# Optimization experiments

Hardware: AMD Instinct MI355X
Metric: run time of the kernel (lower is better)

Reference implementation:

```python
import jax, jax.numpy as jnp
import numpy as np

B, S, D, H, E = 2, 2048, 1024, 2048, 8
TOP_K = 2
AUX_COEF = 0.01


def setup_inputs() -> dict:
    key = jax.random.key(0)
    ks = jax.random.split(key, 5)
    x = jax.random.normal(ks[0], (B, S, D), jnp.float32)
    Wr = jax.random.normal(ks[1], (E, D), jnp.float32) * 0.02   # router: Linear(D, E) weight [E, D]
    W1 = jax.random.normal(ks[2], (E, H, D), jnp.float32) * 0.02  # per-expert Linear(D, H)
    W2 = jax.random.normal(ks[3], (E, D, H), jnp.float32) * 0.02  # per-expert Linear(H, D)
    W3 = jax.random.normal(ks[4], (E, H, D), jnp.float32) * 0.02  # per-expert Linear(D, H)
    return {"x": x, "Wr": Wr, "W1": W1, "W2": W2, "W3": W3}


def reference(x, Wr, W1, W2, W3):
    b, s, d = x.shape
    e = Wr.shape[0]
    xf = x.reshape(-1, d)                               # [N, D]
    logits = xf @ Wr.T                                  # [N, E]
    probs = jax.nn.softmax(logits, axis=-1)
    _, topk_idx = jax.lax.top_k(logits, TOP_K)          # indices from logits (as in torch code)
    topk_probs, _ = jax.lax.top_k(probs, TOP_K)         # values from probs (same order; softmax monotone)
    # aux loss: density of top-1 expert * mean router prob
    density = jnp.mean(jax.nn.one_hot(topk_idx[:, 0], e, dtype=xf.dtype), axis=0)
    aux_loss = AUX_COEF * jnp.sum(density * probs.mean(axis=0)) * e
    # combine gates: gate[n, j] = sum_i topk_probs[n,i] * 1[topk_idx[n,i]==j]
    gates = jnp.sum(jax.nn.one_hot(topk_idx, e, dtype=xf.dtype) * topk_probs[..., None], axis=1)  # [N, E]
    # dense per-expert SwiGLU; masked combine gives identical math to gather/scatter loop
    h = jax.nn.silu(jnp.einsum('nd,ehd->enh', xf, W1)) * jnp.einsum('nd,ehd->enh', xf, W3)  # [E, N, H]
    y = jnp.einsum('enh,edh->end', h, W2)               # [E, N, D]
    out = jnp.einsum('ne,end->nd', gates, y)            # [N, D]
    return out.reshape(b, s, d), aux_loss
```

## Files before the change

kernel.cpp:

```cpp
#include <hip/hip_runtime.h>
#include <stdint.h>

#define NTOK 4096
#define DD 1024
#define HH 2048
#define NE 8
#define CAP 4096

typedef short bf16x8 __attribute__((ext_vector_type(8)));
typedef float f32x4 __attribute__((ext_vector_type(4)));
typedef unsigned short u16;
typedef unsigned int u32;

__device__ __forceinline__ u16 f2b(float f){
    union { float f; u32 u; } v; v.f = f;
    return (u16)((v.u + 0x7fffu + ((v.u >> 16) & 1u)) >> 16);
}
__device__ __forceinline__ u32 pk2(float a, float b){
    return (u32)f2b(a) | ((u32)f2b(b) << 16);
}
__device__ __forceinline__ void gload16(const u16* g, u16* l){
    __builtin_amdgcn_global_load_lds((const __attribute__((address_space(1))) u32*)g,
                                     (__attribute__((address_space(3))) u32*)l, 16, 0, 0);
}

__global__ __launch_bounds__(256) void cvt_w_kernel(const float* __restrict__ W1,
        const float* __restrict__ W2, const float* __restrict__ W3,
        u16* __restrict__ w1b, u16* __restrict__ w2b, u16* __restrict__ w3b){
    int y = blockIdx.y;
    const float* s; u16* d;
    if (y == 0){ s = W1; d = w1b; }
    else if (y == 1){ s = W2; d = w2b; }
    else { s = W3; d = w3b; }
    int i = blockIdx.x * 256 + threadIdx.x;
    float4 v = reinterpret_cast<const float4*>(s)[i];
    ushort4 o; o.x = f2b(v.x); o.y = f2b(v.y); o.z = f2b(v.z); o.w = f2b(v.w);
    reinterpret_cast<ushort4*>(d)[i] = o;
}

__global__ __launch_bounds__(256) void router_kernel(const float* __restrict__ x,
                              const float* __restrict__ Wr,
                              int* __restrict__ cnt, int* __restrict__ list,
                              float* __restrict__ glist, float* __restrict__ psum,
                              int* __restrict__ cnt1, int* __restrict__ islot,
                              u16* __restrict__ xb){
    __shared__ float wS[NE * DD];
    __shared__ float psumS[NE];
    __shared__ int cnt1S[NE], cntS[NE], baseS[NE];
    __shared__ int tE[32], tL[32];
    __shared__ float tP[32];
    int tid = threadIdx.x;
    for (int i = tid; i < NE * DD / 4; i += 256)
        reinterpret_cast<float4*>(wS)[i] = reinterpret_cast<const float4*>(Wr)[i];
    if (tid < NE){ psumS[tid] = 0.f; cnt1S[tid] = 0; cntS[tid] = 0; }
    __syncthreads();
    int lane = tid & 63, w = tid >> 6;
    for (int t = 0; t < 4; ++t){
        int li = w * 4 + t;
        int n = blockIdx.x * 16 + li;
        const float4* xr = reinterpret_cast<const float4*>(x + (size_t)n * DD);
        ushort4* xbr = reinterpret_cast<ushort4*>(xb + (size_t)n * DD);
        float acc[NE];
        #pragma unroll
        for (int e = 0; e < NE; ++e) acc[e] = 0.f;
        #pragma unroll
        for (int j = 0; j < 4; ++j){
            float4 xv = xr[lane + 64 * j];
            ushort4 xo; xo.x = f2b(xv.x); xo.y = f2b(xv.y); xo.z = f2b(xv.z); xo.w = f2b(xv.w);
            xbr[lane + 64 * j] = xo;
            #pragma unroll
            for (int e = 0; e < NE; ++e){
                float4 wv = reinterpret_cast<const float4*>(wS + e * DD)[lane + 64 * j];
                acc[e] += xv.x * wv.x + xv.y * wv.y + xv.z * wv.z + xv.w * wv.w;
            }
        }
        #pragma unroll
        for (int e = 0; e < NE; ++e){
            float v = acc[e];
            #pragma unroll
            for (int s = 32; s > 0; s >>= 1) v += __shfl_xor(v, s);
            acc[e] = v;
        }
        if (lane == 0){
            float mx = acc[0];
            #pragma unroll
            for (int e = 1; e < NE; ++e) mx = fmaxf(mx, acc[e]);
            float p[NE], sm = 0.f;
            #pragma unroll
            for (int e = 0; e < NE; ++e){ p[e] = expf(acc[e] - mx); sm += p[e]; }
            float inv = 1.f / sm;
            #pragma unroll
            for (int e = 0; e < NE; ++e){ p[e] *= inv; atomicAdd(&psumS[e], p[e]); }
            int i0 = 0;
            #pragma unroll
            for (int e = 1; e < NE; ++e) if (acc[e] > acc[i0]) i0 = e;
            int i1 = -1;
            #pragma unroll
            for (int e = 0; e < NE; ++e) if (e != i0 && (i1 < 0 || acc[e] > acc[i1])) i1 = e;
            atomicAdd(&cnt1S[i0], 1);
            int l0 = atomicAdd(&cntS[i0], 1);
            int l1 = atomicAdd(&cntS[i1], 1);
            tE[li * 2] = i0; tE[li * 2 + 1] = i1;
            tP[li * 2] = p[i0]; tP[li * 2 + 1] = p[i1];
            tL[li * 2] = l0; tL[li * 2 + 1] = l1;
        }
    }
    __syncthreads();
    if (tid < NE){
        baseS[tid] = atomicAdd(&cnt[tid], cntS[tid]);
        atomicAdd(&psum[tid], psumS[tid]);
        atomicAdd(&cnt1[tid], cnt1S[tid]);
    }
    __syncthreads();
    if (tid < 32){
        int e = tE[tid], pos = baseS[e] + tL[tid];
        int n = blockIdx.x * 16 + (tid >> 1);
        list[e * CAP + pos]  = n;
        glist[e * CAP + pos] = tP[tid];
        islot[n * 2 + (tid & 1)] = e * CAP + pos;
    }
}

__global__ void finalize_kernel(const int* __restrict__ cnt, int* __restrict__ offs,
                                const float* __restrict__ psum, const int* __restrict__ cnt1,
                                float* __restrict__ aux_out){
    if (threadIdx.x == 0 && blockIdx.x == 0){
        int o = 0; float aux = 0.f;
        for (int e = 0; e < NE; ++e){
            offs[e] = o; o += cnt[e];
            aux += ((float)cnt1[e] * (1.f / NTOK)) * (psum[e] * (1.f / NTOK));
        }
        aux_out[0] = 0.01f * aux * (float)NE;
    }
}

__global__ __launch_bounds__(256, 3) void ffn1_kernel(const u16* __restrict__ xb,
        const u16* __restrict__ w1b, const u16* __restrict__ w3b,
        const int* __restrict__ cnt, const int* __restrict__ offs,
        const int* __restrict__ list, u16* __restrict__ hbuf){
    int bid = blockIdx.x;
    int widx = (bid & 7) * 1024 + (bid >> 3);
    int e = widx >> 10, n0t = (widx >> 5) & 31, mt = widx & 31;
    int rows = cnt[e];
    int m0 = mt * 128;
    if (m0 >= rows) return;
    int n0 = n0t * 64;

    __shared__ u16 aS[128 * 64];
    __shared__ u16 bS[128 * 64];

    int tid = threadIdx.x, lane = tid & 63, w = tid >> 6;
    int wm = (w & 1) * 64, wn = (w >> 1) * 32;
    int fr = lane & 15, fg = lane >> 4, fr7 = fr & 7;
    int rc = lane >> 3, ce = ((lane & 7) ^ rc) * 8;

    const u16* aptr[4];
    const u16* bptr[4];
    #pragma unroll
    for (int q = 0; q < 4; ++q){
        int r = m0 + (w * 4 + q) * 8 + rc;
        int tok = list[e * CAP + (r < rows ? r : rows - 1)];
        aptr[q] = xb + (size_t)tok * DD + ce;
        int br = (w * 4 + q) * 8 + rc;
        const u16* wb = (br < 64) ? w1b : w3b;
        bptr[q] = wb + ((size_t)e * HH + n0 + (br & 63)) * DD + ce;
    }
    u16* aL = aS + w * 4 * 512;
    u16* bL = bS + w * 4 * 512;

    f32x4 acc1[4][2], acc3[4][2];
    #pragma unroll
    for (int mi = 0; mi < 4; ++mi)
        #pragma unroll
        for (int ni = 0; ni < 2; ++ni)
            #pragma unroll
            for (int j = 0; j < 4; ++j){ acc1[mi][ni][j] = 0.f; acc3[mi][ni][j] = 0.f; }

    for (int k0 = 0; k0 < DD; k0 += 64){
        #pragma unroll
        for (int q = 0; q < 4; ++q){
            gload16(aptr[q] + k0, aL + q * 512);
            gload16(bptr[q] + k0, bL + q * 512);
        }
        __syncthreads();
        #pragma unroll
        for (int ks = 0; ks < 2; ++ks){
            int sl = ((ks * 4 + fg) ^ fr7) * 8;
            bf16x8 a[4], b1[2], b3[2];
            #pragma unroll
            for (int mi = 0; mi < 4; ++mi)
                a[mi] = *reinterpret_cast<const bf16x8*>(&aS[(wm + mi * 16 + fr) * 64 + sl]);
            #pragma unroll
            for (int ni = 0; ni < 2; ++ni){
                b1[ni] = *reinterpret_cast<const bf16x8*>(&bS[(wn + ni * 16 + fr) * 64 + sl]);
                b3[ni] = *reinterpret_cast<const bf16x8*>(&bS[(64 + wn + ni * 16 + fr) * 64 + sl]);
            }
            #pragma unroll
            for (int mi = 0; mi < 4; ++mi)
                #pragma unroll
                for (int ni = 0; ni < 2; ++ni){
                    acc1[mi][ni] = __builtin_amdgcn_mfma_f32_16x16x32_bf16(a[mi], b1[ni], acc1[mi][ni], 0, 0, 0);
                    acc3[mi][ni] = __builtin_amdgcn_mfma_f32_16x16x32_bf16(a[mi], b3[ni], acc3[mi][ni], 0, 0, 0);
                }
        }
        __syncthreads();
    }

    int hoff = offs[e];
    #pragma unroll
    for (int mi = 0; mi < 4; ++mi)
        #pragma unroll
        for (int ni = 0; ni < 2; ++ni)
            #pragma unroll
            for (int j = 0; j < 4; ++j){
                int r = wm + mi * 16 + fg * 4 + j;
                int tr = m0 + r;
                if (tr < rows){
                    int c = n0 + wn + ni * 16 + fr;
                    float v1 = acc1[mi][ni][j], v3 = acc3[mi][ni][j];
                    float hv = (v1 / (1.f + expf(-v1))) * v3;
                    hbuf[(size_t)(hoff + tr) * HH + c] = f2b(hv);
                }
            }
}

__global__ __launch_bounds__(256, 3) void ffn2_kernel(const u16* __restrict__ hbuf,
        const u16* __restrict__ w2b, const int* __restrict__ cnt,
        const int* __restrict__ offs, float* __restrict__ ybuf){
    int bid = blockIdx.x;
    int widx = (bid & 7) * 256 + (bid >> 3);
    int e = widx >> 8, n0t = (widx >> 5) & 7, mt = widx & 31;
    int rows = cnt[e];
    int m0 = mt * 128;
    if (m0 >= rows) return;
    int n0 = n0t * 128;

    __shared__ u16 aS[128 * 64];
    __shared__ u16 bS[128 * 64];

    int tid = threadIdx.x, lane = tid & 63, w = tid >> 6;
    int wm = (w & 1) * 64, wn = (w >> 1) * 64;
    int fr = lane & 15, fg = lane >> 4, fr7 = fr & 7;
    int rc = lane >> 3, ce = ((lane & 7) ^ rc) * 8;

    int hoff = offs[e];
    const u16* aptr[4];
    #pragma unroll
    for (int q = 0; q < 4; ++q){
        int r = m0 + (w * 4 + q) * 8 + rc;
        if (r >= rows) r = rows - 1;
        aptr[q] = hbuf + (size_t)(hoff + r) * HH + ce;
    }
    const u16* bp = w2b + ((size_t)e * DD + n0 + w * 32 + rc) * HH + ce;
    u16* aL = aS + w * 4 * 512;
    u16* bL = bS + w * 4 * 512;

    f32x4 acc[4][4];
    #pragma unroll
    for (int mi = 0; mi < 4; ++mi)
        #pragma unroll
        for (int ni = 0; ni < 4; ++ni)
            #pragma unroll
            for (int j = 0; j < 4; ++j) acc[mi][ni][j] = 0.f;

    for (int k0 = 0; k0 < HH; k0 += 64){
        #pragma unroll
        for (int q = 0; q < 4; ++q){
            gload16(aptr[q] + k0, aL + q * 512);
            gload16(bp + q * 8 * HH + k0, bL + q * 512);
        }
        __syncthreads();
        #pragma unroll
        for (int ks = 0; ks < 2; ++ks){
            int sl = ((ks * 4 + fg) ^ fr7) * 8;
            bf16x8 a[4], b[4];
            #pragma unroll
            for (int mi = 0; mi < 4; ++mi)
                a[mi] = *reinterpret_cast<const bf16x8*>(&aS[(wm + mi * 16 + fr) * 64 + sl]);
            #pragma unroll
            for (int ni = 0; ni < 4; ++ni)
                b[ni] = *reinterpret_cast<const bf16x8*>(&bS[(wn + ni * 16 + fr) * 64 + sl]);
            #pragma unroll
            for (int mi = 0; mi < 4; ++mi)
                #pragma unroll
                for (int ni = 0; ni < 4; ++ni)
                    acc[mi][ni] = __builtin_amdgcn_mfma_f32_16x16x32_bf16(a[mi], b[ni], acc[mi][ni], 0, 0, 0);
        }
        __syncthreads();
    }

    #pragma unroll
    for (int mi = 0; mi < 4; ++mi)
        #pragma unroll
        for (int ni = 0; ni < 4; ++ni)
            #pragma unroll
            for (int j = 0; j < 4; ++j){
                int r = wm + mi * 16 + fg * 4 + j;
                int tr = m0 + r;
                if (tr < rows){
                    int c = wn + ni * 16 + fr;
                    ybuf[(size_t)(hoff + tr) * DD + n0 + c] = acc[mi][ni][j];
                }
            }
}

__global__ __launch_bounds__(256, 2) void ffn1_small(const u16* __restrict__ xb,
        const float* __restrict__ W1f, const float* __restrict__ W3f,
        const int* __restrict__ cnt, const int* __restrict__ offs,
        const int* __restrict__ list, u16* __restrict__ hbuf){
    int bid = blockIdx.x;
    int widx = (bid & 7) * 512 + (bid >> 3);
    int e = widx >> 9, n0t = (widx >> 5) & 15, mt = widx & 31;
    int rows = cnt[e];
    int m0 = mt * 128;
    if (m0 >= rows) return;
    int n0 = n0t * 128;
    __shared__ u16 aS[128 * 64];
    __shared__ u16 b1S[128 * 64];
    __shared__ u16 b3S[128 * 64];
    int tid = threadIdx.x, lane = tid & 63, w = tid >> 6;
    int wm = (w & 1) * 64, wn = (w >> 1) * 64;
    int fr = lane & 15, fg = lane >> 4, fr7 = fr & 7;
    int rc = lane >> 3, ce = ((lane & 7) ^ rc) * 8;
    const u16* aptr[4];
    #pragma unroll
    for (int q = 0; q < 4; ++q){
        int r = m0 + (w * 4 + q) * 8 + rc;
        int tok = list[e * CAP + (r < rows ? r : rows - 1)];
        aptr[q] = xb + (size_t)tok * DD + ce;
    }
    size_t brw = (size_t)(e * HH + n0 + w * 32 + rc) * DD + ce;
    const float* b1pf = W1f + brw;
    const float* b3pf = W3f + brw;
    u16* aL  = aS  + w * 4 * 512;
    u16* b1L = b1S + w * 4 * 512;
    u16* b3L = b3S + w * 4 * 512;
    f32x4 acc1[4][4], acc3[4][4];
    #pragma unroll
    for (int mi = 0; mi < 4; ++mi)
        #pragma unroll
        for (int ni = 0; ni < 4; ++ni)
            #pragma unroll
            for (int j = 0; j < 4; ++j){ acc1[mi][ni][j] = 0.f; acc3[mi][ni][j] = 0.f; }
    for (int k0 = 0; k0 < DD; k0 += 64){
        #pragma unroll
        for (int q = 0; q < 4; ++q){
            gload16(aptr[q] + k0, aL + q * 512);
            const float* s1 = b1pf + q * 8 * DD + k0;
            float4 f0 = reinterpret_cast<const float4*>(s1)[0];
            float4 f1 = reinterpret_cast<const float4*>(s1)[1];
            int4 v; v.x = pk2(f0.x,f0.y); v.y = pk2(f0.z,f0.w); v.z = pk2(f1.x,f1.y); v.w = pk2(f1.z,f1.w);
            *reinterpret_cast<int4*>(b1L + q * 512 + lane * 8) = v;
            const float* s3 = b3pf + q * 8 * DD + k0;
            float4 g0 = reinterpret_cast<const float4*>(s3)[0];
            float4 g1 = reinterpret_cast<const float4*>(s3)[1];
            int4 u; u.x = pk2(g0.x,g0.y); u.y = pk2(g0.z,g0.w); u.z = pk2(g1.x,g1.y); u.w = pk2(g1.z,g1.w);
            *reinterpret_cast<int4*>(b3L + q * 512 + lane * 8) = u;
        }
        __syncthreads();
        #pragma unroll
        for (int ks = 0; ks < 2; ++ks){
            int sl = ((ks * 4 + fg) ^ fr7) * 8;
            bf16x8 a[4], b1[4], b3[4];
            #pragma unroll
            for (int mi = 0; mi < 4; ++mi)
                a[mi] = *reinterpret_cast<const bf16x8*>(&aS[(wm + mi * 16 + fr) * 64 + sl]);
            #pragma unroll
            for (int ni = 0; ni < 4; ++ni){
                b1[ni] = *reinterpret_cast<const bf16x8*>(&b1S[(wn + ni * 16 + fr) * 64 + sl]);
                b3[ni] = *reinterpret_cast<const bf16x8*>(&b3S[(wn + ni * 16 + fr) * 64 + sl]);
            }
            #pragma unroll
            for (int mi = 0; mi < 4; ++mi)
                #pragma unroll
                for (int ni = 0; ni < 4; ++ni){
                    acc1[mi][ni] = __builtin_amdgcn_mfma_f32_16x16x32_bf16(a[mi], b1[ni], acc1[mi][ni], 0, 0, 0);
                    acc3[mi][ni] = __builtin_amdgcn_mfma_f32_16x16x32_bf16(a[mi], b3[ni], acc3[mi][ni], 0, 0, 0);
                }
        }
        __syncthreads();
    }
    int hoff = offs[e];
    #pragma unroll
    for (int mi = 0; mi < 4; ++mi)
        #pragma unroll
        for (int ni = 0; ni < 4; ++ni)
            #pragma unroll
            for (int j = 0; j < 4; ++j){
                int r = wm + mi * 16 + fg * 4 + j;
                int tr = m0 + r;
                if (tr < rows){
                    int c = wn + ni * 16 + fr;
                    float v1 = acc1[mi][ni][j], v3 = acc3[mi][ni][j];
                    float hv = (v1 / (1.f + expf(-v1))) * v3;
                    hbuf[(size_t)(hoff + tr) * HH + n0 + c] = f2b(hv);
                }
            }
}

__global__ __launch_bounds__(256, 2) void ffn2_small(const u16* __restrict__ hbuf,
        const float* __restrict__ W2f, const int* __restrict__ cnt,
        const int* __restrict__ offs, float* __restrict__ ybuf){
    int bid = blockIdx.x;
    int widx = (bid & 7) * 256 + (bid >> 3);
    int e = widx >> 8, n0t = (widx >> 5) & 7, mt = widx & 31;
    int rows = cnt[e];
    int m0 = mt * 128;
    if (m0 >= rows) return;
    int n0 = n0t * 128;
    __shared__ u16 aS[128 * 64];
    __shared__ u16 bS[128 * 64];
    int tid = threadIdx.x, lane = tid & 63, w = tid >> 6;
    int wm = (w & 1) * 64, wn = (w >> 1) * 64;
    int fr = lane & 15, fg = lane >> 4, fr7 = fr & 7;
    int rc = lane >> 3, ce = ((lane & 7) ^ rc) * 8;
    int hoff = offs[e];
    const u16* aptr[4];
    #pragma unroll
    for (int q = 0; q < 4; ++q){
        int r = m0 + (w * 4 + q) * 8 + rc;
        if (r >= rows) r = rows - 1;
        aptr[q] = hbuf + (size_t)(hoff + r) * HH + ce;
    }
    const float* b2pf = W2f + (size_t)(e * DD + n0 + w * 32 + rc) * HH + ce;
    u16* aL = aS + w * 4 * 512;
    u16* bL = bS + w * 4 * 512;
    f32x4 acc[4][4];
    #pragma unroll
    for (int mi = 0; mi < 4; ++mi)
        #pragma unroll
        for (int ni = 0; ni < 4; ++ni)
            #pragma unroll
            for (int j = 0; j < 4; ++j) acc[mi][ni][j] = 0.f;
    for (int k0 = 0; k0 < HH; k0 += 64){
        #pragma unroll
        for (int q = 0; q < 4; ++q){
            gload16(aptr[q] + k0, aL + q * 512);
            const float* s2 = b2pf + q * 8 * HH + k0;
            float4 f0 = reinterpret_cast<const float4*>(s2)[0];
            float4 f1 = reinterpret_cast<const float4*>(s2)[1];
            int4 v; v.x = pk2(f0.x,f0.y); v.y = pk2(f0.z,f0.w); v.z = pk2(f1.x,f1.y); v.w = pk2(f1.z,f1.w);
            *reinterpret_cast<int4*>(bL + q * 512 + lane * 8) = v;
        }
        __syncthreads();
        #pragma unroll
        for (int ks = 0; ks < 2; ++ks){
            int sl = ((ks * 4 + fg) ^ fr7) * 8;
            bf16x8 a[4], b[4];
            #pragma unroll
            for (int mi = 0; mi < 4; ++mi)
                a[mi] = *reinterpret_cast<const bf16x8*>(&aS[(wm + mi * 16 + fr) * 64 + sl]);
            #pragma unroll
            for (int ni = 0; ni < 4; ++ni)
                b[ni] = *reinterpret_cast<const bf16x8*>(&bS[(wn + ni * 16 + fr) * 64 + sl]);
            #pragma unroll
            for (int mi = 0; mi < 4; ++mi)
                #pragma unroll
                for (int ni = 0; ni < 4; ++ni)
                    acc[mi][ni] = __builtin_amdgcn_mfma_f32_16x16x32_bf16(a[mi], b[ni], acc[mi][ni], 0, 0, 0);
        }
        __syncthreads();
    }
    #pragma unroll
    for (int mi = 0; mi < 4; ++mi)
        #pragma unroll
        for (int ni = 0; ni < 4; ++ni)
            #pragma unroll
            for (int j = 0; j < 4; ++j){
                int r = wm + mi * 16 + fg * 4 + j;
                int tr = m0 + r;
                if (tr < rows){
                    int c = wn + ni * 16 + fr;
                    ybuf[(size_t)(hoff + tr) * DD + n0 + c] = acc[mi][ni][j];
                }
            }
}

__global__ __launch_bounds__(256) void combine_kernel(const float* __restrict__ ybuf,
        const int* __restrict__ islot, const int* __restrict__ offs,
        const float* __restrict__ glist, float* __restrict__ out){
    int idx = blockIdx.x * 256 + threadIdx.x;
    int n = idx >> 7, c = (idx & 127) * 8;
    int id0 = islot[n * 2], id1 = islot[n * 2 + 1];
    int r0 = offs[id0 >> 12] + (id0 & 4095);
    int r1 = offs[id1 >> 12] + (id1 & 4095);
    float g0 = glist[id0], g1 = glist[id1];
    const float4* y0 = reinterpret_cast<const float4*>(ybuf + (size_t)r0 * DD + c);
    const float4* y1 = reinterpret_cast<const float4*>(ybuf + (size_t)r1 * DD + c);
    float4 a0 = y0[0], a1 = y0[1], b0 = y1[0], b1 = y1[1];
    float4 o0, o1;
    o0.x = g0 * a0.x + g1 * b0.x; o0.y = g0 * a0.y + g1 * b0.y;
    o0.z = g0 * a0.z + g1 * b0.z; o0.w = g0 * a0.w + g1 * b0.w;
    o1.x = g0 * a1.x + g1 * b1.x; o1.y = g0 * a1.y + g1 * b1.y;
    o1.z = g0 * a1.z + g1 * b1.z; o1.w = g0 * a1.w + g1 * b1.w;
    float4* op = reinterpret_cast<float4*>(out + (size_t)n * DD + c);
    op[0] = o0; op[1] = o1;
}

extern "C" void kernel_launch(void* const* d_in, const int* in_sizes, int n_in,
                              void* d_out, int out_size, void* d_ws, size_t ws_size,
                              hipStream_t stream) {
    const float* x  = (const float*)d_in[0];
    const float* Wr = (const float*)d_in[1];
    const float* W1 = (const float*)d_in[2];
    const float* W2 = (const float*)d_in[3];
    const float* W3 = (const float*)d_in[4];
    float* out = (float*)d_out;

    char* wp = (char*)d_ws;
    u16*   hbuf  = (u16*)  (wp);
    u16*   xb    = (u16*)  (wp + 33554432);
    int*   list  = (int*)  (wp + 41943040);
    float* glist = (float*)(wp + 42074112);
    int*   cnt   = (int*)  (wp + 42205184);
    int*   offs  = (int*)  (wp + 42205216);
    float* psum  = (float*)(wp + 42205248);
    int*   cnt1  = (int*)  (wp + 42205280);
    int*   islot = (int*)  (wp + 42205312);
    const size_t WOFF = 42238208;
    const size_t WB   = 33554432;
    u16* w1b = (u16*)(wp + WOFF);
    u16* w2b = (u16*)(wp + WOFF + WB);
    u16* w3b = (u16*)(wp + WOFF + 2 * WB);
    float* ybuf = (float*)(wp + WOFF);
    const size_t NEED_FULL = WOFF + 3 * WB;
    bool bw = ws_size >= NEED_FULL;

    hipMemsetAsync(wp + 42205184, 0, 128, stream);

    if (bw)
        cvt_w_kernel<<<dim3(NE * HH * DD / 4 / 256, 3), 256, 0, stream>>>(
            W1, W2, W3, w1b, w2b, w3b);
    router_kernel<<<NTOK / 16, 256, 0, stream>>>(x, Wr, cnt, list, glist, psum, cnt1, islot, xb);
    finalize_kernel<<<1, 64, 0, stream>>>(cnt, offs, psum, cnt1, out + (size_t)NTOK * DD);
    if (bw){
        ffn1_kernel<<<8192, 256, 0, stream>>>(xb, w1b, w3b, cnt, offs, list, hbuf);
        ffn2_kernel<<<2048, 256, 0, stream>>>(hbuf, w2b, cnt, offs, ybuf);
    } else {
        ffn1_small<<<4096, 256, 0, stream>>>(xb, W1, W3, cnt, offs, list, hbuf);
        ffn2_small<<<2048, 256, 0, stream>>>(hbuf, W2, cnt, offs, ybuf);
    }
    combine_kernel<<<NTOK * (DD / 8) / 256, 256, 0, stream>>>(ybuf, islot, offs, glist, out);
}
```

Baseline: 239.8 us.

## Double-buffer LDS tiles in ffn1 and ffn2 to overlap global loads with MFMA

Both grouped GEMM kernels now allocate two LDS stages and issue the direct-to-LDS global loads for the next K tile before running MFMAs on the current one. This keeps memory fetches in flight during compute instead of stalling on them each iteration, and it leaves one barrier per iteration. In exchange, LDS use per block doubles to 64 KB, so launch bounds drop from 3 to 2 blocks per CU and occupancy falls.

After: 290.6 us. 21.2% more time.

```diff
diff --git a/kernel.cpp b/kernel.cpp
--- a/kernel.cpp
+++ b/kernel.cpp
@@ -134,7 +134,7 @@
     }
 }
 
-__global__ __launch_bounds__(256, 3) void ffn1_kernel(const u16* __restrict__ xb,
+__global__ __launch_bounds__(256, 2) void ffn1_kernel(const u16* __restrict__ xb,
         const u16* __restrict__ w1b, const u16* __restrict__ w3b,
         const int* __restrict__ cnt, const int* __restrict__ offs,
         const int* __restrict__ list, u16* __restrict__ hbuf){
@@ -146,8 +146,8 @@
     if (m0 >= rows) return;
     int n0 = n0t * 64;
 
-    __shared__ u16 aS[128 * 64];
-    __shared__ u16 bS[128 * 64];
+    __shared__ u16 aS[2 * 128 * 64];
+    __shared__ u16 bS[2 * 128 * 64];
 
     int tid = threadIdx.x, lane = tid & 63, w = tid >> 6;
     int wm = (w & 1) * 64, wn = (w >> 1) * 32;
@@ -165,8 +165,14 @@
         const u16* wb = (br < 64) ? w1b : w3b;
         bptr[q] = wb + ((size_t)e * HH + n0 + (br & 63)) * DD + ce;
     }
-    u16* aL = aS + w * 4 * 512;
-    u16* bL = bS + w * 4 * 512;
+
+    auto STAGE = [&](u16* Ad, u16* Bd, int kofs){
+        #pragma unroll
+        for (int q = 0; q < 4; ++q){
+            gload16(aptr[q] + kofs, Ad + (w * 4 + q) * 512);
+            gload16(bptr[q] + kofs, Bd + (w * 4 + q) * 512);
+        }
+    };
 
     f32x4 acc1[4][2], acc3[4][2];
     #pragma unroll
@@ -176,24 +182,30 @@
             #pragma unroll
             for (int j = 0; j < 4; ++j){ acc1[mi][ni][j] = 0.f; acc3[mi][ni][j] = 0.f; }
 
-    for (int k0 = 0; k0 < DD; k0 += 64){
-        #pragma unroll
-        for (int q = 0; q < 4; ++q){
-            gload16(aptr[q] + k0, aL + q * 512);
-            gload16(bptr[q] + k0, bL + q * 512);
-        }
-        __syncthreads();
+    const int NT = DD / 64;
+    STAGE(aS, bS, 0);
+    asm volatile("s_waitcnt vmcnt(0)" ::: "memory");
+    __builtin_amdgcn_s_barrier();
+    __builtin_amdgcn_sched_barrier(0);
+
+    for (int t = 0; t < NT; ++t){
+        int cur = t & 1;
+        u16* Ac = aS + cur * 8192;
+        u16* Bc = bS + cur * 8192;
+        if (t + 1 < NT)
+            STAGE(aS + (cur ^ 1) * 8192, bS + (cur ^ 1) * 8192, (t + 1) * 64);
+
         #pragma unroll
         for (int ks = 0; ks < 2; ++ks){
             int sl = ((ks * 4 + fg) ^ fr7) * 8;
             bf16x8 a[4], b1[2], b3[2];
             #pragma unroll
             for (int mi = 0; mi < 4; ++mi)
-                a[mi] = *reinterpret_cast<const bf16x8*>(&aS[(wm + mi * 16 + fr) * 64 + sl]);
+                a[mi] = *reinterpret_cast<const bf16x8*>(&Ac[(wm + mi * 16 + fr) * 64 + sl]);
             #pragma unroll
             for (int ni = 0; ni < 2; ++ni){
-                b1[ni] = *reinterpret_cast<const bf16x8*>(&bS[(wn + ni * 16 + fr) * 64 + sl]);
-                b3[ni] = *reinterpret_cast<const bf16x8*>(&bS[(64 + wn + ni * 16 + fr) * 64 + sl]);
+                b1[ni] = *reinterpret_cast<const bf16x8*>(&Bc[(wn + ni * 16 + fr) * 64 + sl]);
+                b3[ni] = *reinterpret_cast<const bf16x8*>(&Bc[(64 + wn + ni * 16 + fr) * 64 + sl]);
             }
             #pragma unroll
             for (int mi = 0; mi < 4; ++mi)
@@ -203,7 +215,9 @@
                     acc3[mi][ni] = __builtin_amdgcn_mfma_f32_16x16x32_bf16(a[mi], b3[ni], acc3[mi][ni], 0, 0, 0);
                 }
         }
-        __syncthreads();
+        asm volatile("s_waitcnt vmcnt(0) lgkmcnt(0)" ::: "memory");
+        __builtin_amdgcn_s_barrier();
+        __builtin_amdgcn_sched_barrier(0);
     }
 
     int hoff = offs[e];
@@ -224,7 +238,7 @@
             }
 }
 
-__global__ __launch_bounds__(256, 3) void ffn2_kernel(const u16* __restrict__ hbuf,
+__global__ __launch_bounds__(256, 2) void ffn2_kernel(const u16* __restrict__ hbuf,
         const u16* __restrict__ w2b, const int* __restrict__ cnt,
         const int* __restrict__ offs, float* __restrict__ ybuf){
     int bid = blockIdx.x;
@@ -235,8 +249,8 @@
     if (m0 >= rows) return;
     int n0 = n0t * 128;
 
-    __shared__ u16 aS[128 * 64];
-    __shared__ u16 bS[128 * 64];
+    __shared__ u16 aS[2 * 128 * 64];
+    __shared__ u16 bS[2 * 128 * 64];
 
     int tid = threadIdx.x, lane = tid & 63, w = tid >> 6;
     int wm = (w & 1) * 64, wn = (w >> 1) * 64;
@@ -252,8 +266,14 @@
         aptr[q] = hbuf + (size_t)(hoff + r) * HH + ce;
     }
     const u16* bp = w2b + ((size_t)e * DD + n0 + w * 32 + rc) * HH + ce;
-    u16* aL = aS + w * 4 * 512;
-    u16* bL = bS + w * 4 * 512;
+
+    auto STAGE = [&](u16* Ad, u16* Bd, int kofs){
+        #pragma unroll
+        for (int q = 0; q < 4; ++q){
+            gload16(aptr[q] + kofs, Ad + (w * 4 + q) * 512);
+            gload16(bp + q * 8 * HH + kofs, Bd + (w * 4 + q) * 512);
+        }
+    };
 
     f32x4 acc[4][4];
     #pragma unroll
@@ -263,30 +283,38 @@
             #pragma unroll
             for (int j = 0; j < 4; ++j) acc[mi][ni][j] = 0.f;
 
-    for (int k0 = 0; k0 < HH; k0 += 64){
-        #pragma unroll
-        for (int q = 0; q < 4; ++q){
-            gload16(aptr[q] + k0, aL + q * 512);
-            gload16(bp + q * 8 * HH + k0, bL + q * 512);
-        }
-        __syncthreads();
+    const int NT = HH / 64;
+    STAGE(aS, bS, 0);
+    asm volatile("s_waitcnt vmcnt(0)" ::: "memory");
+    __builtin_amdgcn_s_barrier();
+    __builtin_amdgcn_sched_barrier(0);
+
+    for (int t = 0; t < NT; ++t){
+        int cur = t & 1;
+        u16* Ac = aS + cur * 8192;
+        u16* Bc = bS + cur * 8192;
+        if (t + 1 < NT)
+            STAGE(aS + (cur ^ 1) * 8192, bS + (cur ^ 1) * 8192, (t + 1) * 64);
+
         #pragma unroll
         for (int ks = 0; ks < 2; ++ks){
             int sl = ((ks * 4 + fg) ^ fr7) * 8;
             bf16x8 a[4], b[4];
             #pragma unroll
             for (int mi = 0; mi < 4; ++mi)
-                a[mi] = *reinterpret_cast<const bf16x8*>(&aS[(wm + mi * 16 + fr) * 64 + sl]);
+                a[mi] = *reinterpret_cast<const bf16x8*>(&Ac[(wm + mi * 16 + fr) * 64 + sl]);
             #pragma unroll
             for (int ni = 0; ni < 4; ++ni)
-                b[ni] = *reinterpret_cast<const bf16x8*>(&bS[(wn + ni * 16 + fr) * 64 + sl]);
+                b[ni] = *reinterpret_cast<const bf16x8*>(&Bc[(wn + ni * 16 + fr) * 64 + sl]);
             #pragma unroll
             for (int mi = 0; mi < 4; ++mi)
                 #pragma unroll
                 for (int ni = 0; ni < 4; ++ni)
                     acc[mi][ni] = __builtin_amdgcn_mfma_f32_16x16x32_bf16(a[mi], b[ni], acc[mi][ni], 0, 0, 0);
         }
-        __syncthreads();
+        asm volatile("s_waitcnt vmcnt(0) lgkmcnt(0)" ::: "memory");
+        __builtin_amdgcn_s_barrier();
+        __builtin_amdgcn_sched_barrier(0);
     }
 
     #pragma unroll
```
